# Optimization experiments

Hardware: AMD Instinct MI355X
Metric: run time of the kernel (lower is better)

## Reference

```python
import jax, jax.numpy as jnp
import numpy as np

TEMP = 0.07
WEIGHT = 0.5
EPS = 1e-8  # matches torch F.cosine_similarity norm clamp


def setup_inputs() -> dict:
    key = jax.random.key(0)
    k1, k2, k3 = jax.random.split(key, 3)
    B, T, D = 64, 512, 512
    video = jax.random.normal(k1, (B, T, D), dtype=jnp.float32)
    audio = jax.random.normal(k2, (B, T, D), dtype=jnp.float32)
    mask = jax.random.randint(k3, (B, T), 0, 2, dtype=jnp.int32)
    return {"video": video, "audio": audio, "mask": mask}


def reference(video, audio, mask):
    B, T, D = video.shape
    # L2-normalize features (cosine similarity = dot of normalized vectors)
    vn = video / jnp.clip(jnp.linalg.norm(video, axis=-1, keepdims=True), EPS)
    an = audio / jnp.clip(jnp.linalg.norm(audio, axis=-1, keepdims=True), EPS)
    idx = jnp.argmax(mask, axis=1)                                   # [B]
    a_anchor = jnp.take_along_axis(an, idx[:, None, None], axis=1)[:, 0]  # [B,D]
    v_anchor = jnp.take_along_axis(vn, idx[:, None, None], axis=1)[:, 0]  # [B,D]
    # scaled cosine sims of all timesteps vs the anchor of the other modality
    sims_a2v = jnp.einsum('btd,bd->bt', vn, a_anchor) / TEMP         # cos(v_j, a_idx)/T
    sims_v2a = jnp.einsum('btd,bd->bt', an, v_anchor) / TEMP         # cos(a_j, v_idx)/T
    # positive: cos(v_idx, a_idx)/T (same for both directions)
    pos = jnp.take_along_axis(sims_a2v, idx[:, None], axis=1)[:, 0]  # [B]
    not_pos = jnp.arange(T)[None, :] != idx[:, None]                 # [B,T]
    neg_a = jnp.sum(jnp.where(not_pos, jnp.exp(sims_a2v), 0.0), axis=1)  # a2v negatives
    neg_v = jnp.sum(jnp.where(not_pos, jnp.exp(sims_v2a), 0.0), axis=1)  # v2a negatives
    pos_exp = jnp.exp(pos)
    batch_loss_a = jnp.sum(-jnp.log(pos_exp / neg_a))
    batch_loss_v = jnp.sum(-jnp.log(pos_exp / neg_v))
    return ((batch_loss_a * WEIGHT + batch_loss_v * WEIGHT) / B).reshape(1)
```

## Files before the change

### kernel.cpp

```cpp
#include <hip/hip_runtime.h>
#include <math.h>

#define TEMP_INV (1.0f / 0.07f)
#define WEIGHT 0.5f
#define EPS 1e-8f
#define BB 64
#define TT 512
#define DD 512
#define RR 4
#define NC 4
#define ROWS_PER_WAVE (RR * NC)

typedef float f32x4 __attribute__((ext_vector_type(4)));

__device__ inline float wave_sum(float v) {
    for (int o = 32; o >= 1; o >>= 1) v += __shfl_xor(v, o, 64);
    return v;
}
__device__ inline int wave_max_i(int v) {
    for (int o = 32; o >= 1; o >>= 1) v = max(v, __shfl_xor(v, o, 64));
    return v;
}
__device__ inline int wave_min_i(int v) {
    for (int o = 32; o >= 1; o >>= 1) v = min(v, __shfl_xor(v, o, 64));
    return v;
}

__global__ __launch_bounds__(256) void prep_kernel(
    const float* __restrict__ video, const float* __restrict__ audio,
    const int* __restrict__ mask,
    float* __restrict__ a_anchor, float* __restrict__ v_anchor,
    float* __restrict__ pos, float* __restrict__ neg, int* __restrict__ idx_out)
{
    const int b = blockIdx.x;
    const int tid = threadIdx.x;
    const int wid = tid >> 6, lane = tid & 63;
    __shared__ int sh_i[4];
    __shared__ float sh_f[4][3];
    __shared__ int s_idx;
    __shared__ float s_inva, s_invv;

    int m0 = mask[b * TT + tid];
    int m1 = mask[b * TT + tid + 256];
    int vmax = wave_max_i(max(m0, m1));
    if (lane == 0) sh_i[wid] = vmax;
    __syncthreads();
    if (tid == 0) {
        int r = sh_i[0];
        for (int i = 1; i < 4; i++) r = max(r, sh_i[i]);
        sh_i[0] = r;
    }
    __syncthreads();
    vmax = sh_i[0];
    __syncthreads();
    int cand = (m0 == vmax) ? tid : 0x7fffffff;
    int cand1 = (m1 == vmax) ? (tid + 256) : 0x7fffffff;
    cand = min(cand, cand1);
    cand = wave_min_i(cand);
    if (lane == 0) sh_i[wid] = cand;
    __syncthreads();
    if (tid == 0) {
        int r = sh_i[0];
        for (int i = 1; i < 4; i++) r = min(r, sh_i[i]);
        s_idx = r;
    }
    __syncthreads();
    const int idx = s_idx;

    const float* arow = audio + ((size_t)(b * TT + idx)) * DD;
    const float* vrow = video + ((size_t)(b * TT + idx)) * DD;
    float a0 = arow[tid], a1 = arow[tid + 256];
    float v0 = vrow[tid], v1 = vrow[tid + 256];
    float ssa = a0 * a0 + a1 * a1;
    float ssv = v0 * v0 + v1 * v1;
    float dav = a0 * v0 + a1 * v1;
    ssa = wave_sum(ssa);
    ssv = wave_sum(ssv);
    dav = wave_sum(dav);
    if (lane == 0) { sh_f[wid][0] = ssa; sh_f[wid][1] = ssv; sh_f[wid][2] = dav; }
    __syncthreads();
    if (tid == 0) {
        float ra = 0.f, rv = 0.f, rd = 0.f;
        for (int i = 0; i < 4; i++) { ra += sh_f[i][0]; rv += sh_f[i][1]; rd += sh_f[i][2]; }
        float inva = 1.0f / fmaxf(sqrtf(ra), EPS);
        float invv = 1.0f / fmaxf(sqrtf(rv), EPS);
        s_inva = inva; s_invv = invv;
        pos[b] = rd * inva * invv * TEMP_INV;
        neg[b] = 0.0f;
        neg[BB + b] = 0.0f;
        idx_out[b] = idx;
    }
    __syncthreads();
    const float inva = s_inva, invv = s_invv;
    a_anchor[b * DD + tid] = a0 * inva;
    a_anchor[b * DD + tid + 256] = a1 * inva;
    v_anchor[b * DD + tid] = v0 * invv;
    v_anchor[b * DD + tid + 256] = v1 * invv;
}

#define LOADC(B0, B1, CH)                                                   \
    _Pragma("unroll")                                                       \
    for (int r = 0; r < RR; r++) {                                          \
        const float* row_ = base + (size_t)(t0 + (CH) * RR + r) * DD;       \
        B0[r] = *(const f32x4*)(row_ + lane * 4);                           \
        B1[r] = *(const f32x4*)(row_ + 256 + lane * 4);                     \
    }

#define COMPC(B0, B1, CH)                                                   \
    _Pragma("unroll")                                                       \
    for (int r = 0; r < RR; r++) {                                          \
        const int k_ = (CH) * RR + r;                                       \
        dot[k_] = B0[r].x * c0.x + B0[r].y * c0.y + B0[r].z * c0.z          \
                + B0[r].w * c0.w + B1[r].x * c1.x + B1[r].y * c1.y          \
                + B1[r].z * c1.z + B1[r].w * c1.w;                          \
        nrm[k_] = B0[r].x * B0[r].x + B0[r].y * B0[r].y + B0[r].z * B0[r].z \
                + B0[r].w * B0[r].w + B1[r].x * B1[r].x + B1[r].y * B1[r].y \
                + B1[r].z * B1[r].z + B1[r].w * B1[r].w;                    \
    }

__global__ __launch_bounds__(256) void sims_kernel(
    const float* __restrict__ video, const float* __restrict__ audio,
    const float* __restrict__ a_anchor, const float* __restrict__ v_anchor,
    const int* __restrict__ idx_arr, float* __restrict__ neg)
{
    const int b = blockIdx.y;
    const int dir = blockIdx.z;
    const int wid = threadIdx.x >> 6, lane = threadIdx.x & 63;
    const int t0 = blockIdx.x * (4 * ROWS_PER_WAVE) + wid * ROWS_PER_WAVE;

    const float* base = (dir == 0 ? video : audio) + (size_t)b * TT * DD;
    const float* anc = (dir == 0 ? a_anchor : v_anchor) + b * DD;

    f32x4 c0 = *(const f32x4*)(anc + lane * 4);
    f32x4 c1 = *(const f32x4*)(anc + 256 + lane * 4);

    f32x4 pa0[RR], pa1[RR], pb0[RR], pb1[RR];
    float dot[ROWS_PER_WAVE], nrm[ROWS_PER_WAVE];

    LOADC(pa0, pa1, 0)
    LOADC(pb0, pb1, 1)
    COMPC(pa0, pa1, 0)
    LOADC(pa0, pa1, 2)
    COMPC(pb0, pb1, 1)
    LOADC(pb0, pb1, 3)
    COMPC(pa0, pa1, 2)
    COMPC(pb0, pb1, 3)

#pragma unroll
    for (int o = 32; o >= 1; o >>= 1) {
#pragma unroll
        for (int k = 0; k < ROWS_PER_WAVE; k++) {
            dot[k] += __shfl_xor(dot[k], o, 64);
            nrm[k] += __shfl_xor(nrm[k], o, 64);
        }
    }

    if (lane == 0) {
        const int idx = idx_arr[b];
        float local = 0.0f;
#pragma unroll
        for (int k = 0; k < ROWS_PER_WAVE; k++) {
            const int t = t0 + k;
            float sim = dot[k] / fmaxf(sqrtf(nrm[k]), EPS) * TEMP_INV;
            local += (t == idx) ? 0.0f : expf(sim);
        }
        atomicAdd(&neg[dir * BB + b], local);
    }
}

__global__ void finalize_kernel(const float* __restrict__ pos,
                                const float* __restrict__ neg,
                                float* __restrict__ out)
{
    const int b = threadIdx.x;
    float term = WEIGHT * (logf(neg[b]) + logf(neg[BB + b])) - pos[b];
    term = wave_sum(term);
    if (b == 0) out[0] = term / (float)BB;
}

extern "C" void kernel_launch(void* const* d_in, const int* in_sizes, int n_in,
                              void* d_out, int out_size, void* d_ws, size_t ws_size,
                              hipStream_t stream)
{
    const float* video = (const float*)d_in[0];
    const float* audio = (const float*)d_in[1];
    const int* mask = (const int*)d_in[2];

    float* ws = (float*)d_ws;
    float* a_anchor = ws;
    float* v_anchor = ws + BB * DD;
    float* pos = ws + 2 * BB * DD;
    float* neg = pos + BB;
    int* idx = (int*)(neg + 2 * BB);

    prep_kernel<<<BB, 256, 0, stream>>>(video, audio, mask, a_anchor, v_anchor, pos, neg, idx);
    dim3 grid(TT / (4 * ROWS_PER_WAVE), BB, 2);
    sims_kernel<<<grid, 256, 0, stream>>>(video, audio, a_anchor, v_anchor, idx, neg);
    finalize_kernel<<<1, 64, 0, stream>>>(pos, neg, (float*)d_out);
}
```

Measured before the change: 158.9 us.

## Fuse prep, sims and finalize into one kernel with last-block reduction

Merges the three launches into a single kernel. Each block recomputes the anchor index from the mask and the anchor norm itself, and per-block partial sums go to a workspace array. The last block to arrive, detected through an atomic counter, does the final log-sum reduction. This removes two kernel launches, the inter-kernel gaps and the global anchor round-trip, in exchange for redundant mask scans and anchor loads in every block plus a memset launch. The pos values are written with relaxed atomics and read back by the last block, and there is no explicit release/acquire fence on that path.

```diff
diff --git a/kernel.cpp b/kernel.cpp
--- a/kernel.cpp
+++ b/kernel.cpp
@@ -10,6 +10,8 @@
 #define RR 4
 #define NC 4
 #define ROWS_PER_WAVE (RR * NC)
+#define XBLK (TT / (4 * ROWS_PER_WAVE))
+#define NBLK (XBLK * BB * 2)
 
 typedef float f32x4 __attribute__((ext_vector_type(4)));
 
@@ -24,78 +26,6 @@
 __device__ inline int wave_min_i(int v) {
     for (int o = 32; o >= 1; o >>= 1) v = min(v, __shfl_xor(v, o, 64));
     return v;
-}
-
-__global__ __launch_bounds__(256) void prep_kernel(
-    const float* __restrict__ video, const float* __restrict__ audio,
-    const int* __restrict__ mask,
-    float* __restrict__ a_anchor, float* __restrict__ v_anchor,
-    float* __restrict__ pos, float* __restrict__ neg, int* __restrict__ idx_out)
-{
-    const int b = blockIdx.x;
-    const int tid = threadIdx.x;
-    const int wid = tid >> 6, lane = tid & 63;
-    __shared__ int sh_i[4];
-    __shared__ float sh_f[4][3];
-    __shared__ int s_idx;
-    __shared__ float s_inva, s_invv;
-
-    int m0 = mask[b * TT + tid];
-    int m1 = mask[b * TT + tid + 256];
-    int vmax = wave_max_i(max(m0, m1));
-    if (lane == 0) sh_i[wid] = vmax;
-    __syncthreads();
-    if (tid == 0) {
-        int r = sh_i[0];
-        for (int i = 1; i < 4; i++) r = max(r, sh_i[i]);
-        sh_i[0] = r;
-    }
-    __syncthreads();
-    vmax = sh_i[0];
-    __syncthreads();
-    int cand = (m0 == vmax) ? tid : 0x7fffffff;
-    int cand1 = (m1 == vmax) ? (tid + 256) : 0x7fffffff;
-    cand = min(cand, cand1);
-    cand = wave_min_i(cand);
-    if (lane == 0) sh_i[wid] = cand;
-    __syncthreads();
-    if (tid == 0) {
-        int r = sh_i[0];
-        for (int i = 1; i < 4; i++) r = min(r, sh_i[i]);
-        s_idx = r;
-    }
-    __syncthreads();
-    const int idx = s_idx;
-
-    const float* arow = audio + ((size_t)(b * TT + idx)) * DD;
-    const float* vrow = video + ((size_t)(b * TT + idx)) * DD;
-    float a0 = arow[tid], a1 = arow[tid + 256];
-    float v0 = vrow[tid], v1 = vrow[tid + 256];
-    float ssa = a0 * a0 + a1 * a1;
-    float ssv = v0 * v0 + v1 * v1;
-    float dav = a0 * v0 + a1 * v1;
-    ssa = wave_sum(ssa);
-    ssv = wave_sum(ssv);
-    dav = wave_sum(dav);
-    if (lane == 0) { sh_f[wid][0] = ssa; sh_f[wid][1] = ssv; sh_f[wid][2] = dav; }
-    __syncthreads();
-    if (tid == 0) {
-        float ra = 0.f, rv = 0.f, rd = 0.f;
-        for (int i = 0; i < 4; i++) { ra += sh_f[i][0]; rv += sh_f[i][1]; rd += sh_f[i][2]; }
-        float inva = 1.0f / fmaxf(sqrtf(ra), EPS);
-        float invv = 1.0f / fmaxf(sqrtf(rv), EPS);
-        s_inva = inva; s_invv = invv;
-        pos[b] = rd * inva * invv * TEMP_INV;
-        neg[b] = 0.0f;
-        neg[BB + b] = 0.0f;
-        idx_out[b] = idx;
-    }
-    __syncthreads();
-    const float inva = s_inva, invv = s_invv;
-    a_anchor[b * DD + tid] = a0 * inva;
-    a_anchor[b * DD + tid + 256] = a1 * inva;
-    v_anchor[b * DD + tid] = v0 * invv;
-    v_anchor[b * DD + tid + 256] = v1 * invv;
 }
 
 #define LOADC(B0, B1, CH)                                                   \
@@ -118,21 +48,87 @@
                 + B1[r].z * B1[r].z + B1[r].w * B1[r].w;                    \
     }
 
-__global__ __launch_bounds__(256) void sims_kernel(
+__global__ __launch_bounds__(256) void fused_kernel(
     const float* __restrict__ video, const float* __restrict__ audio,
-    const float* __restrict__ a_anchor, const float* __restrict__ v_anchor,
-    const int* __restrict__ idx_arr, float* __restrict__ neg)
+    const int* __restrict__ mask,
+    float* __restrict__ pos, float* __restrict__ part,
+    unsigned int* __restrict__ counter, float* __restrict__ out)
 {
     const int b = blockIdx.y;
     const int dir = blockIdx.z;
-    const int wid = threadIdx.x >> 6, lane = threadIdx.x & 63;
+    const int tid = threadIdx.x;
+    const int wid = tid >> 6, lane = tid & 63;
     const int t0 = blockIdx.x * (4 * ROWS_PER_WAVE) + wid * ROWS_PER_WAVE;
 
+    __shared__ int sh_i[4];
+    __shared__ float sh_f[4][3];
+    __shared__ int s_idx;
+    __shared__ float s_anc[DD];
+    __shared__ float s_inv;
+    __shared__ int s_last;
+
+    int m0 = mask[b * TT + tid];
+    int m1 = mask[b * TT + tid + 256];
+    int vmax = wave_max_i(max(m0, m1));
+    if (lane == 0) sh_i[wid] = vmax;
+    __syncthreads();
+    if (tid == 0) {
+        int r = sh_i[0];
+        for (int i = 1; i < 4; i++) r = max(r, sh_i[i]);
+        sh_i[0] = r;
+    }
+    __syncthreads();
+    vmax = sh_i[0];
+    __syncthreads();
+    int cand = (m0 == vmax) ? tid : 0x7fffffff;
+    int cand1 = (m1 == vmax) ? (tid + 256) : 0x7fffffff;
+    cand = min(cand, cand1);
+    cand = wave_min_i(cand);
+    if (lane == 0) sh_i[wid] = cand;
+    __syncthreads();
+    if (tid == 0) {
+        int r = sh_i[0];
+        for (int i = 1; i < 4; i++) r = min(r, sh_i[i]);
+        s_idx = r;
+    }
+    __syncthreads();
+    const int idx = s_idx;
+
     const float* base = (dir == 0 ? video : audio) + (size_t)b * TT * DD;
-    const float* anc = (dir == 0 ? a_anchor : v_anchor) + b * DD;
-
-    f32x4 c0 = *(const f32x4*)(anc + lane * 4);
-    f32x4 c1 = *(const f32x4*)(anc + 256 + lane * 4);
+    const float* ancrow = (dir == 0 ? audio : video) + (size_t)(b * TT + idx) * DD;
+
+    float a0 = ancrow[tid], a1 = ancrow[tid + 256];
+    s_anc[tid] = a0;
+    s_anc[tid + 256] = a1;
+    float ss = a0 * a0 + a1 * a1;
+    float sso = 0.0f, dav = 0.0f;
+    const bool posduty = (blockIdx.x == 0) && (dir == 0);
+    if (posduty) {
+        const float* vrow = video + (size_t)(b * TT + idx) * DD;
+        float o0 = vrow[tid], o1 = vrow[tid + 256];
+        sso = o0 * o0 + o1 * o1;
+        dav = a0 * o0 + a1 * o1;
+    }
+    ss = wave_sum(ss);
+    sso = wave_sum(sso);
+    dav = wave_sum(dav);
+    if (lane == 0) { sh_f[wid][0] = ss; sh_f[wid][1] = sso; sh_f[wid][2] = dav; }
+    __syncthreads();
+    if (tid == 0) {
+        float ra = 0.f, ro = 0.f, rd = 0.f;
+        for (int i = 0; i < 4; i++) { ra += sh_f[i][0]; ro += sh_f[i][1]; rd += sh_f[i][2]; }
+        float inva = 1.0f / fmaxf(sqrtf(ra), EPS);
+        s_inv = inva;
+        if (posduty) {
+            float invo = 1.0f / fmaxf(sqrtf(ro), EPS);
+            __hip_atomic_store(&pos[b], rd * inva * invo * TEMP_INV,
+                               __ATOMIC_RELAXED, __HIP_MEMORY_SCOPE_AGENT);
+        }
+    }
+    __syncthreads();
+    const float inv = s_inv;
+    f32x4 c0 = ((const f32x4*)s_anc)[lane] * inv;
+    f32x4 c1 = ((const f32x4*)(s_anc + 256))[lane] * inv;
 
     f32x4 pa0[RR], pa1[RR], pb0[RR], pb1[RR];
     float dot[ROWS_PER_WAVE], nrm[ROWS_PER_WAVE];
@@ -156,26 +152,44 @@
     }
 
     if (lane == 0) {
-        const int idx = idx_arr[b];
+        const int idx2 = idx;
         float local = 0.0f;
 #pragma unroll
         for (int k = 0; k < ROWS_PER_WAVE; k++) {
             const int t = t0 + k;
             float sim = dot[k] / fmaxf(sqrtf(nrm[k]), EPS) * TEMP_INV;
-            local += (t == idx) ? 0.0f : expf(sim);
+            local += (t == idx2) ? 0.0f : expf(sim);
         }
-        atomicAdd(&neg[dir * BB + b], local);
-    }
-}
-
-__global__ void finalize_kernel(const float* __restrict__ pos,
-                                const float* __restrict__ neg,
-                                float* __restrict__ out)
-{
-    const int b = threadIdx.x;
-    float term = WEIGHT * (logf(neg[b]) + logf(neg[BB + b])) - pos[b];
-    term = wave_sum(term);
-    if (b == 0) out[0] = term / (float)BB;
+        sh_f[wid][0] = local;
+    }
+    __syncthreads();
+    if (tid == 0) {
+        float p = sh_f[0][0] + sh_f[1][0] + sh_f[2][0] + sh_f[3][0];
+        const int bid_flat = (dir * BB + b) * XBLK + blockIdx.x;
+        __hip_atomic_store(&part[bid_flat], p,
+                           __ATOMIC_RELAXED, __HIP_MEMORY_SCOPE_AGENT);
+        asm volatile("s_waitcnt vmcnt(0)" ::: "memory");
+        unsigned old = __hip_atomic_fetch_add(counter, 1u,
+                                              __ATOMIC_RELAXED, __HIP_MEMORY_SCOPE_AGENT);
+        s_last = (old == (unsigned)(NBLK - 1)) ? 1 : 0;
+    }
+    __syncthreads();
+    if (s_last && wid == 0) {
+        float na = 0.f, nv = 0.f;
+#pragma unroll
+        for (int x = 0; x < XBLK; x++)
+            na += __hip_atomic_load(&part[(0 * BB + lane) * XBLK + x],
+                                    __ATOMIC_RELAXED, __HIP_MEMORY_SCOPE_AGENT);
+#pragma unroll
+        for (int x = 0; x < XBLK; x++)
+            nv += __hip_atomic_load(&part[(1 * BB + lane) * XBLK + x],
+                                    __ATOMIC_RELAXED, __HIP_MEMORY_SCOPE_AGENT);
+        float p = __hip_atomic_load(&pos[lane],
+                                    __ATOMIC_RELAXED, __HIP_MEMORY_SCOPE_AGENT);
+        float term = WEIGHT * (logf(na) + logf(nv)) - p;
+        term = wave_sum(term);
+        if (lane == 0) out[0] = term * (1.0f / (float)BB);
+    }
 }
 
 extern "C" void kernel_launch(void* const* d_in, const int* in_sizes, int n_in,
@@ -187,14 +201,12 @@
     const int* mask = (const int*)d_in[2];
 
     float* ws = (float*)d_ws;
-    float* a_anchor = ws;
-    float* v_anchor = ws + BB * DD;
-    float* pos = ws + 2 * BB * DD;
-    float* neg = pos + BB;
-    int* idx = (int*)(neg + 2 * BB);
-
-    prep_kernel<<<BB, 256, 0, stream>>>(video, audio, mask, a_anchor, v_anchor, pos, neg, idx);
-    dim3 grid(TT / (4 * ROWS_PER_WAVE), BB, 2);
-    sims_kernel<<<grid, 256, 0, stream>>>(video, audio, a_anchor, v_anchor, idx, neg);
-    finalize_kernel<<<1, 64, 0, stream>>>(pos, neg, (float*)d_out);
-}
+    float* pos = ws;
+    float* part = ws + BB;
+    unsigned int* counter = (unsigned int*)(part + NBLK);
+
+    hipMemsetAsync(counter, 0, sizeof(unsigned int), stream);
+
+    dim3 grid(XBLK, BB, 2);
+    fused_kernel<<<grid, 256, 0, stream>>>(video, audio, mask, pos, part, counter, (float*)d_out);
+}
```

Measured after the change: 153.4 us. -3.5%, faster.
